# Kernel tuning notes

Measured on AMD Instinct MI355X. Metric: run time of the kernel, lower is better.

The kernel has to match this reference:

```python
import jax, jax.numpy as jnp
import numpy as np

QK_NOPE = 128  # qk_nope_head_dim; softmax scale uses nope+rope head dim
EPS = 1e-6

def _rmsnorm(x, w):
    return x * jax.lax.rsqrt(jnp.mean(x * x, axis=-1, keepdims=True) + EPS) * w

def _deinterleave(x):
    # torch: view(..., d//2, 2).transpose(-1, -2).reshape(..., d)
    return jnp.concatenate([x[..., 0::2], x[..., 1::2]], axis=-1)

def _rotate_half(x):
    h = x.shape[-1] // 2
    return jnp.concatenate([-x[..., h:], x[..., :h]], axis=-1)

def _rope_cos_sin(position_ids, dim, theta=10000.0):
    inv_freq = 1.0 / (theta ** (jnp.arange(0, dim, 2, dtype=jnp.float32) / dim))  # [dim/2]
    freqs = position_ids.astype(jnp.float32)[..., None] * inv_freq               # [B,S,dim/2]
    emb = jnp.concatenate([freqs, freqs], axis=-1)                               # [B,S,dim]
    return jnp.cos(emb)[:, None], jnp.sin(emb)[:, None]                          # [B,1,S,dim]


def setup_inputs() -> dict:
    B, S, HID, H = 2, 1024, 4096, 32
    QL, KVL, ROPE, V = 1536, 512, 64, 128
    key = jax.random.key(0)
    ks = jax.random.split(key, 8)
    def w(k, shape, fan_in):
        return jax.random.normal(k, shape, jnp.float32) * (fan_in ** -0.5)
    hidden_states = jax.random.normal(ks[0], (B, S, HID), jnp.float32)
    causal = jnp.tril(jnp.ones((S, S), bool))
    attention_mask = jnp.where(causal, 0.0, -1e9).astype(jnp.float32)[None, None]  # [1,1,S,S]
    position_ids = jnp.broadcast_to(jnp.arange(S, dtype=jnp.int32), (B, S))
    return {
        'hidden_states': hidden_states,
        'attention_mask': attention_mask,
        'position_ids': position_ids,
        'w_q_a': w(ks[1], (HID, QL), HID),
        'q_a_ln_w': jnp.ones((QL,), jnp.float32),
        'q_rope': w(ks[2], (QL, H * ROPE), QL),
        'fusedqk': w(ks[3], (H, QL, KVL), QL),
        'w_kv_a': w(ks[4], (HID, KVL + ROPE), HID),
        'kv_a_ln_w': jnp.ones((KVL,), jnp.float32),
        'per_head_v_up': w(ks[5], (H, KVL, V), KVL),
        'w_o': w(ks[6], (H * V, HID), H * V),
    }


def _mla_forward(hidden_states, attention_mask, position_ids, w_q_a, q_a_ln_w,
                 q_rope, fusedqk, w_kv_a, kv_a_ln_w, per_head_v_up, w_o):
    B, S, _ = hidden_states.shape
    H, QL, KVL = fusedqk.shape
    ROPE = q_rope.shape[1] // H
    # compressed KV projection (MQA): split into latent kv and rope key part
    ckv = hidden_states @ w_kv_a                              # [B,S,KVL+ROPE]
    kva = _rmsnorm(ckv[..., :KVL], kv_a_ln_w)                 # [B,S,KVL]
    k_pe = ckv[..., KVL:][:, None]                            # [B,1,S,ROPE]
    # low-rank query
    q_a = _rmsnorm(hidden_states @ w_q_a, q_a_ln_w)           # [B,S,QL]
    q_pe = (q_a @ q_rope).reshape(B, S, H, ROPE).transpose(0, 2, 1, 3)  # [B,H,S,ROPE]
    # interleaved RoPE (deinterleave then standard rotate-half)
    cos, sin = _rope_cos_sin(position_ids, ROPE)
    qd = _deinterleave(q_pe)
    kd = _deinterleave(k_pe)
    q_pe = qd * cos + _rotate_half(qd) * sin                  # [B,H,S,ROPE]
    k_pe = kd * cos + _rotate_half(kd) * sin                  # [B,1,S,ROPE]
    # absorbed query: q_a @ (q_up @ k_up^T), precomputed as fusedqk
    q_abs = jnp.einsum('bsr,hrc->bhsc', q_a, fusedqk)         # [B,H,S,KVL]
    query = jnp.concatenate([q_abs, q_pe], axis=-1)           # [B,H,S,KVL+ROPE]
    keys = jnp.concatenate([kva, k_pe[:, 0]], axis=-1)        # [B,S,KVL+ROPE]
    scale = (QK_NOPE + ROPE) ** -0.5
    scores = jnp.einsum('bhsd,btd->bhst', query, keys) * scale + attention_mask
    attn = jax.nn.softmax(scores, axis=-1)                    # [B,H,S,S]
    ctx = jnp.einsum('bhst,btc->bhsc', attn, kva)             # [B,H,S,KVL]
    out = jnp.einsum('bhsc,hcv->bhsv', ctx, per_head_v_up)    # [B,H,S,V]
    out = out.transpose(0, 2, 1, 3).reshape(B, S, -1)         # [B,S,H*V]
    return out @ w_o                                          # [B,S,HID]


def reference(hidden_states, attention_mask, position_ids, w_q_a, q_a_ln_w,
              q_rope, fusedqk, w_kv_a, kv_a_ln_w, per_head_v_up, w_o):
    return _mla_forward(hidden_states, attention_mask, position_ids, w_q_a,
                        q_a_ln_w, q_rope, fusedqk, w_kv_a, kv_a_ln_w,
                        per_head_v_up, w_o)
```

## Files before the change

### kernel.cpp

```cpp
#include <hip/hip_runtime.h>


typedef __attribute__((ext_vector_type(8))) short s16x8;
typedef __attribute__((ext_vector_type(4))) float f32x4;

__device__ __forceinline__ float bf2f(unsigned short u) {
  union { unsigned int i; float f; } v; v.i = ((unsigned int)u) << 16; return v.f;
}
__device__ __forceinline__ unsigned short f2bf(float f) {
  union { float f; unsigned int i; } v; v.f = f;
  unsigned int x = v.i;
  x += 0x7fffu + ((x >> 16) & 1u);
  return (unsigned short)(x >> 16);
}

__device__ __forceinline__ void async16(const unsigned short* g, unsigned short* l) {
  __builtin_amdgcn_global_load_lds(
      (const __attribute__((address_space(1))) unsigned int*)g,
      (__attribute__((address_space(3))) unsigned int*)l, 16, 0, 0);
}

__global__ __launch_bounds__(256) void conv_bf16(
    const float* __restrict__ s, unsigned short* __restrict__ d)
{
  const long long i = ((long long)blockIdx.x * 256 + threadIdx.x) * 8;
  float4 a = *(const float4*)(s + i);
  float4 b = *(const float4*)(s + i + 4);
  union { uint4 v; unsigned short u[8]; } o;
  o.u[0] = f2bf(a.x); o.u[1] = f2bf(a.y); o.u[2] = f2bf(a.z); o.u[3] = f2bf(a.w);
  o.u[4] = f2bf(b.x); o.u[5] = f2bf(b.y); o.u[6] = f2bf(b.z); o.u[7] = f2bf(b.w);
  *(uint4*)(d + i) = o.v;
}

__global__ __launch_bounds__(256) void transpose_w(
    const float* __restrict__ src, unsigned short* __restrict__ dst,
    int R, int C, long long sS, long long sD)
{
  __shared__ unsigned short tile[32][36];
  src += (long long)blockIdx.z * sS;
  dst += (long long)blockIdx.z * sD;
  const int c0 = blockIdx.x * 32, r0 = blockIdx.y * 32;
  const int tid = threadIdx.x;
  const int rr = tid >> 3, cc4 = (tid & 7) * 4;
  if (c0 < C) {
    float4 v = *(const float4*)(src + (long long)(r0 + rr) * C + c0 + cc4);
    tile[cc4 + 0][rr] = f2bf(v.x); tile[cc4 + 1][rr] = f2bf(v.y);
    tile[cc4 + 2][rr] = f2bf(v.z); tile[cc4 + 3][rr] = f2bf(v.w);
  } else {
#pragma unroll
    for (int j = 0; j < 4; ++j) tile[cc4 + j][rr] = 0;
  }
  __syncthreads();
  const int cr = tid >> 3, rc4 = (tid & 7) * 4;
  union { uint2 v; unsigned short u[4]; } o;
#pragma unroll
  for (int j = 0; j < 4; ++j) o.u[j] = tile[cr][rc4 + j];
  *(uint2*)(dst + (long long)(c0 + cr) * R + r0 + rc4) = o.v;
}

template<int ODT>
__global__ __launch_bounds__(256) void gemm128(
    const unsigned short* __restrict__ A, const unsigned short* __restrict__ Bt,
    void* __restrict__ Cv, int K, int lda, int ldb, int ldc, int batH,
    long long sAb, long long sAh, long long sBb, long long sBh,
    long long sCb, long long sCh)
{
  const int z = blockIdx.z;
  const int bz = z / batH, hz = z % batH;
  A  += (long long)bz * sAb + (long long)hz * sAh;
  Bt += (long long)bz * sBb + (long long)hz * sBh;
  const long long co = (long long)bz * sCb + (long long)hz * sCh;

  __shared__ __align__(16) unsigned short As[128 * 32];
  __shared__ __align__(16) unsigned short Bs[128 * 32];

  const int tid = threadIdx.x, w = tid >> 6, lane = tid & 63;
  const int quad = lane >> 4, ml = lane & 15;
  const int wm = (w >> 1) * 64, wn = (w & 1) * 64;
  const int m0 = blockIdx.y * 128, n0 = blockIdx.x * 128;

  const int r0 = tid >> 2, k8 = (tid & 3) * 8;
  const unsigned short* Ag0 = A  + (long long)(m0 + r0)      * lda + k8;
  const unsigned short* Ag1 = A  + (long long)(m0 + r0 + 64) * lda + k8;
  const unsigned short* Bg0 = Bt + (long long)(n0 + r0)      * ldb + k8;
  const unsigned short* Bg1 = Bt + (long long)(n0 + r0 + 64) * ldb + k8;
  unsigned short* la0 = &As[tid * 8];
  unsigned short* la1 = &As[(tid + 256) * 8];
  unsigned short* lb0 = &Bs[tid * 8];
  unsigned short* lb1 = &Bs[(tid + 256) * 8];

  f32x4 acc[4][4] = {};

  for (int k0 = 0; k0 < K; k0 += 32) {
    __syncthreads();
    async16(Ag0 + k0, la0);
    async16(Ag1 + k0, la1);
    async16(Bg0 + k0, lb0);
    async16(Bg1 + k0, lb1);
    __syncthreads();

    s16x8 af[4], bf[4];
#pragma unroll
    for (int mi = 0; mi < 4; ++mi)
      af[mi] = *(const s16x8*)(&As[(wm + mi * 16 + ml) * 32 + quad * 8]);
#pragma unroll
    for (int ni = 0; ni < 4; ++ni)
      bf[ni] = *(const s16x8*)(&Bs[(wn + ni * 16 + ml) * 32 + quad * 8]);
#pragma unroll
    for (int mi = 0; mi < 4; ++mi)
#pragma unroll
      for (int ni = 0; ni < 4; ++ni)
        acc[mi][ni] = __builtin_amdgcn_mfma_f32_16x16x32_bf16(af[mi], bf[ni], acc[mi][ni], 0, 0, 0);
  }

#pragma unroll
  for (int mi = 0; mi < 4; ++mi)
#pragma unroll
    for (int ni = 0; ni < 4; ++ni)
#pragma unroll
      for (int r = 0; r < 4; ++r) {
        const int row = m0 + wm + mi * 16 + quad * 4 + r;
        const int col = n0 + wn + ni * 16 + ml;
        if (ODT)
          ((unsigned short*)Cv)[co + (long long)row * ldc + col] = f2bf(acc[mi][ni][r]);
        else
          ((float*)Cv)[co + (long long)row * ldc + col] = acc[mi][ni][r];
      }
}

__global__ __launch_bounds__(256) void kv_norm_rope(
    const float* __restrict__ qckv, const float* __restrict__ w,
    const int* __restrict__ pos_ids, unsigned short* __restrict__ keys)
{
  __shared__ float sbuf[4];
  const int r = blockIdx.x, tid = threadIdx.x;
  const float* row = qckv + (long long)r * 2176 + 1536;
  float x0 = row[tid], x1 = row[256 + tid];
  float ss = x0 * x0 + x1 * x1;
#pragma unroll
  for (int o = 32; o; o >>= 1) ss += __shfl_xor(ss, o);
  if ((tid & 63) == 0) sbuf[tid >> 6] = ss;
  __syncthreads();
  const float tot = sbuf[0] + sbuf[1] + sbuf[2] + sbuf[3];
  const float rms = rsqrtf(tot / 512.0f + 1e-6f);
  unsigned short* kr = keys + (long long)r * 576;
  kr[tid]       = f2bf(x0 * rms * w[tid]);
  kr[256 + tid] = f2bf(x1 * rms * w[256 + tid]);
  if (tid < 32) {
    const float pos = (float)pos_ids[r];
    const float invf = exp2f(-0.41524101186098287f * (float)tid);
    float sn, c; sincosf(pos * invf, &sn, &c);
    const float a0 = row[512 + 2 * tid], a1 = row[512 + 2 * tid + 1];
    kr[512 + tid] = f2bf(a0 * c - a1 * sn);
    kr[544 + tid] = f2bf(a1 * c + a0 * sn);
  }
}

__global__ __launch_bounds__(256) void q_norm(
    const float* __restrict__ qckv, const float* __restrict__ w,
    unsigned short* __restrict__ qa_bf)
{
  __shared__ float sbuf[4];
  const int r = blockIdx.x, tid = threadIdx.x;
  const float* row = qckv + (long long)r * 2176;
  float x[6]; float ss = 0.f;
#pragma unroll
  for (int j = 0; j < 6; ++j) { x[j] = row[tid + 256 * j]; ss += x[j] * x[j]; }
#pragma unroll
  for (int o = 32; o; o >>= 1) ss += __shfl_xor(ss, o);
  if ((tid & 63) == 0) sbuf[tid >> 6] = ss;
  __syncthreads();
  const float tot = sbuf[0] + sbuf[1] + sbuf[2] + sbuf[3];
  const float rms = rsqrtf(tot / 1536.0f + 1e-6f);
#pragma unroll
  for (int j = 0; j < 6; ++j) {
    const int idx = tid + 256 * j;
    qa_bf[(long long)r * 1536 + idx] = f2bf(x[j] * rms * w[idx]);
  }
}

__global__ __launch_bounds__(256) void rope_q(
    const unsigned short* __restrict__ qpe, const int* __restrict__ pos_ids,
    unsigned short* __restrict__ query)
{
  const int r = blockIdx.x;
  const int b = r >> 10, s = r & 1023;
  const float pos = (float)pos_ids[r];
  for (int p = threadIdx.x; p < 1024; p += 256) {
    const int h = p >> 5, i = p & 31;
    const float invf = exp2f(-0.41524101186098287f * (float)i);
    float sn, c; sincosf(pos * invf, &sn, &c);
    const float a0 = bf2f(qpe[(long long)r * 2048 + h * 64 + 2 * i]);
    const float a1 = bf2f(qpe[(long long)r * 2048 + h * 64 + 2 * i + 1]);
    const long long qrow = ((long long)(b * 32 + h) * 1024 + s) * 576;
    query[qrow + 512 + i] = f2bf(a0 * c - a1 * sn);
    query[qrow + 544 + i] = f2bf(a1 * c + a0 * sn);
  }
}

__global__ __launch_bounds__(256) void transpose_keys(
    const unsigned short* __restrict__ keys, unsigned short* __restrict__ keysT)
{
  __shared__ unsigned short tile[32][36];
  const int tid = threadIdx.x;
  const int t0 = blockIdx.x * 32, d0 = blockIdx.y * 32, b = blockIdx.z;
  const int r = tid >> 3, c4 = (tid & 7) * 4;
  *(uint2*)(&tile[r][c4]) =
      *(const uint2*)(keys + ((long long)(b * 1024 + t0 + r) * 576 + d0 + c4));
  __syncthreads();
  unsigned short v[4];
#pragma unroll
  for (int j = 0; j < 4; ++j) v[j] = tile[c4 + j][r];
  *(uint2*)(keysT + ((long long)(b * 512 + d0 + r) * 1024 + t0 + c4)) = *(uint2*)v;
}

__global__ __launch_bounds__(512, 2) void flash_mfma(
    const unsigned short* __restrict__ query,
    const unsigned short* __restrict__ keys,
    const unsigned short* __restrict__ keysT,
    unsigned short* __restrict__ ctx)
{
  __shared__ __align__(16) unsigned short Ks[2][32 * 640];
  __shared__ __align__(16) unsigned short Ps[2][8][640];
  __shared__ float alpha_s[2][128];
  __shared__ float l_s[128];
  __shared__ __align__(16) int rflag[2][8];

  const int tid = threadIdx.x, w = tid >> 6, lane = tid & 63;
  const int quad = lane >> 4, ml = lane & 15;
  const int bid = blockIdx.x;
  const int bh = bid & 63;
  const int qt = 7 - (bid >> 6);
  const int q0 = qt * 128;
  const int b = bh >> 5;
  const float scale = 0.07216878364870323f;

  const unsigned short* kb  = keys  + (long long)b * 1024 * 576;
  const unsigned short* vtb = keysT + (long long)b * 512 * 1024;

  const unsigned short* qg =
      query + ((long long)bh * 1024 + q0 + w * 16 + ml) * 576 + quad * 8;
  s16x8 qf[18];
#pragma unroll
  for (int ks = 0; ks < 18; ++ks) qf[ks] = *(const s16x8*)(qg + ks * 32);

  int koff[5];
#pragma unroll
  for (int j = 0; j < 5; ++j) {
    const int idx = tid + 512 * j;
    const int row = idx / 80;
    const int c16 = idx - row * 80;
    koff[j] = row * 576 + ((c16 ^ (row & 7)) << 3);
  }
  char* ldsb = (char*)&Ks[0][0] + tid * 16;
  auto stage = [&](int t, int buf) {
    const long long toff = (long long)t * 18432;
    char* lb = ldsb + buf * 40960;
#pragma unroll
    for (int j = 0; j < 5; ++j)
      async16(kb + toff + koff[j], (unsigned short*)(lb + j * 8192));
  };

  const int e3 = ml & 7;
  const int qi = q0 + w * 16 + ml;
  const int ntile = 4 * qt + 4;

  float m = -1e30f, l = 0.f;
  f32x4 o[8][4] = {};

  stage(0, 0);

  for (int ti = 0; ti < ntile; ++ti) {
    const int buf = ti & 1;
    const int t0 = ti * 32;

    if (ti + 1 < ntile) {
      stage(ti + 1, buf ^ 1);
      asm volatile("s_waitcnt vmcnt(5)" ::: "memory");
    } else {
      asm volatile("s_waitcnt vmcnt(0)" ::: "memory");
    }
    __builtin_amdgcn_sched_barrier(0);
    __builtin_amdgcn_s_barrier();
    __builtin_amdgcn_sched_barrier(0);

    const bool wdead = (t0 > q0 + w * 16 + 15);
    if (!wdead) {
      const unsigned short* Kb = &Ks[buf][0];
      f32x4 sc0 = {}, sc1 = {};
#pragma unroll
      for (int ks = 0; ks < 18; ++ks) {
        const int xr = ((ks * 4 + quad) ^ e3) << 3;
        s16x8 k0 = *(const s16x8*)(Kb + ml * 640 + xr);
        s16x8 k1 = *(const s16x8*)(Kb + (16 + ml) * 640 + xr);
        sc0 = __builtin_amdgcn_mfma_f32_16x16x32_bf16(k0, qf[ks], sc0, 0, 0, 0);
        sc1 = __builtin_amdgcn_mfma_f32_16x16x32_bf16(k1, qf[ks], sc1, 0, 0, 0);
      }

      float p[8]; float mx = -1e30f;
      const bool tail = (t0 + 31 > q0 + w * 16);
#pragma unroll
      for (int r = 0; r < 4; ++r) {
        float v0 = sc0[r] * scale, v1 = sc1[r] * scale;
        if (tail) {
          if (t0 + quad * 4 + r > qi)      v0 = -1e30f;
          if (t0 + 16 + quad * 4 + r > qi) v1 = -1e30f;
        }
        p[r] = v0; p[4 + r] = v1;
        mx = fmaxf(mx, fmaxf(v0, v1));
      }
      mx = fmaxf(mx, __shfl_xor(mx, 16));
      mx = fmaxf(mx, __shfl_xor(mx, 32));

      float alpha = 1.0f;
      int resc = 0;
      if (!__all(mx - m <= 8.0f)) {
        const float mn = fmaxf(m, mx);
        alpha = __expf(m - mn);
        m = mn;
        l *= alpha;
        resc = 1;
      }
      if (lane == 0) rflag[buf][w] = resc;
      if (quad == 0) alpha_s[buf][w * 16 + ml] = alpha;

      float ps = 0.f;
#pragma unroll
      for (int j = 0; j < 8; ++j) { p[j] = __expf(p[j] - m); ps += p[j]; }
      ps += __shfl_xor(ps, 16);
      ps += __shfl_xor(ps, 32);
      l += ps;

#pragma unroll
      for (int c = 0; c < 2; ++c) {
        union { unsigned short u[4]; uint2 v; } pk;
        pk.u[0] = f2bf(p[c * 4 + 0]); pk.u[1] = f2bf(p[c * 4 + 1]);
        pk.u[2] = f2bf(p[c * 4 + 2]); pk.u[3] = f2bf(p[c * 4 + 3]);
        *(uint2*)(&Ps[buf][w][ml * 40 + c * 16 + quad * 4]) = pk.v;
      }
    } else {
      if (lane == 0) rflag[buf][w] = 0;
      if (quad == 0) alpha_s[buf][w * 16 + ml] = 1.0f;
    }

    const unsigned short* vg =
        vtb + (long long)(w * 64 + ml) * 1024 + t0 + quad * 8;
    s16x8 vf[4];
#pragma unroll
    for (int nt = 0; nt < 4; ++nt) vf[nt] = *(const s16x8*)(vg + nt * 16 * 1024);

    asm volatile("s_waitcnt lgkmcnt(0)" ::: "memory");
    __builtin_amdgcn_sched_barrier(0);
    __builtin_amdgcn_s_barrier();
    __builtin_amdgcn_sched_barrier(0);

    const int4 ra = *(const int4*)&rflag[buf][0];
    const int4 rb = *(const int4*)&rflag[buf][4];
    if (ra.x | ra.y | ra.z | ra.w | rb.x | rb.y | rb.z | rb.w) {
#pragma unroll
      for (int qc = 0; qc < 8; ++qc)
#pragma unroll
        for (int r = 0; r < 4; ++r) {
          const float a = alpha_s[buf][qc * 16 + quad * 4 + r];
#pragma unroll
          for (int nt = 0; nt < 4; ++nt) o[qc][nt][r] *= a;
        }
    }

#pragma unroll
    for (int qc = 0; qc < 8; ++qc) {
      if (t0 > q0 + qc * 16 + 15) continue;
      s16x8 pa = *(const s16x8*)(&Ps[buf][qc][ml * 40 + quad * 8]);
#pragma unroll
      for (int nt = 0; nt < 4; ++nt)
        o[qc][nt] = __builtin_amdgcn_mfma_f32_16x16x32_bf16(pa, vf[nt], o[qc][nt], 0, 0, 0);
    }
  }

  if (quad == 0) l_s[w * 16 + ml] = l;
  __syncthreads();

  unsigned short* cb = ctx + ((long long)bh * 1024 + q0) * 512 + w * 64 + ml;
#pragma unroll
  for (int qc = 0; qc < 8; ++qc)
#pragma unroll
    for (int r = 0; r < 4; ++r) {
      const float linv = 1.0f / l_s[qc * 16 + quad * 4 + r];
      unsigned short* crow = cb + (long long)(qc * 16 + quad * 4 + r) * 512;
#pragma unroll
      for (int nt = 0; nt < 4; ++nt)
        crow[nt * 16] = f2bf(o[qc][nt][r] * linv);
    }
}

extern "C" void kernel_launch(void* const* d_in, const int* in_sizes, int n_in,
                              void* d_out, int out_size, void* d_ws, size_t ws_size,
                              hipStream_t stream)
{
  (void)in_sizes; (void)n_in; (void)out_size; (void)ws_size;
  const float* hs      = (const float*)d_in[0];
  const int*   pos     = (const int*)d_in[2];
  const float* w_q_a   = (const float*)d_in[3];
  const float* q_a_ln  = (const float*)d_in[4];
  const float* q_rope  = (const float*)d_in[5];
  const float* fusedqk = (const float*)d_in[6];
  const float* w_kv_a  = (const float*)d_in[7];
  const float* kv_ln   = (const float*)d_in[8];
  const float* v_up    = (const float*)d_in[9];
  const float* w_o     = (const float*)d_in[10];
  char* ws = (char*)d_ws;

  unsigned short* woT    = (unsigned short*)(ws + 0);
  unsigned short* vupT   = (unsigned short*)(ws + 33554432);
  unsigned short* keys   = (unsigned short*)(ws + 37748736);
  unsigned short* keysT  = (unsigned short*)(ws + 40108032);
  unsigned short* ctx    = (unsigned short*)(ws + 42205184);
  unsigned short* fqkT   = (unsigned short*)(ws + 42205184);
  unsigned short* qab    = (unsigned short*)(ws + 92536832);
  unsigned short* qpe    = (unsigned short*)(ws + 99828288);
  unsigned short* hsb    = (unsigned short*)(ws + 92536832);
  unsigned short* query  = (unsigned short*)(ws + 109314048);
  unsigned short* wqkvT  = (unsigned short*)(ws + 109314048);
  unsigned short* qropeT = (unsigned short*)(ws + 127139840);
  float*          qckv   = (float*)(ws + 133431296);
  unsigned short* outh   = (unsigned short*)(ws + 109314048);

  const dim3 blk(256);

  conv_bf16<<<dim3(4096), blk, 0, stream>>>(hs, hsb);
  transpose_w<<<dim3(48, 128, 1), blk, 0, stream>>>(w_q_a, wqkvT, 4096, 1536, 0, 0);
  transpose_w<<<dim3(20, 128, 1), blk, 0, stream>>>(w_kv_a, wqkvT + (long long)1536 * 4096,
      4096, 576, 0, 0);
  transpose_w<<<dim3(64, 48, 1), blk, 0, stream>>>(q_rope, qropeT, 1536, 2048, 0, 0);
  transpose_w<<<dim3(16, 48, 32), blk, 0, stream>>>(fusedqk, fqkT, 1536, 512,
      (long long)1536 * 512, (long long)512 * 1536);
  transpose_w<<<dim3(4, 16, 32), blk, 0, stream>>>(v_up, vupT, 512, 128,
      (long long)512 * 128, (long long)128 * 512);
  transpose_w<<<dim3(128, 128, 1), blk, 0, stream>>>(w_o, woT, 4096, 4096, 0, 0);

  gemm128<0><<<dim3(17, 16, 1), blk, 0, stream>>>(hsb, wqkvT, (void*)qckv,
      4096, 4096, 4096, 2176, 1, 0, 0, 0, 0, 0, 0);
  kv_norm_rope<<<dim3(2048), blk, 0, stream>>>(qckv, kv_ln, pos, keys);
  transpose_keys<<<dim3(32, 16, 2), blk, 0, stream>>>(keys, keysT);
  q_norm<<<dim3(2048), blk, 0, stream>>>(qckv, q_a_ln, qab);
  gemm128<1><<<dim3(16, 16, 1), blk, 0, stream>>>(qab, qropeT, (void*)qpe,
      1536, 1536, 1536, 2048, 1, 0, 0, 0, 0, 0, 0);
  rope_q<<<dim3(2048), blk, 0, stream>>>(qpe, pos, query);
  gemm128<1><<<dim3(4, 8, 64), blk, 0, stream>>>(qab, fqkT, (void*)query,
      1536, 1536, 1536, 576, 32,
      (long long)1024 * 1536, 0, 0, (long long)512 * 1536,
      (long long)32 * 1024 * 576, (long long)1024 * 576);
  flash_mfma<<<dim3(512), dim3(512), 0, stream>>>(query, keys, keysT, ctx);
  gemm128<1><<<dim3(1, 8, 64), blk, 0, stream>>>(ctx, vupT, (void*)outh,
      512, 512, 512, 4096, 32,
      (long long)32 * 1024 * 512, (long long)1024 * 512, 0, (long long)128 * 512,
      (long long)1024 * 4096, 128);
  gemm128<0><<<dim3(32, 16, 1), blk, 0, stream>>>(outh, woT, d_out,
      4096, 4096, 4096, 4096, 1, 0, 0, 0, 0, 0, 0);
}
```

Baseline: 904.9 us.

## Have each wave own its query rows across full latent dim in flash attention

Restructures the PV step so each wave accumulates output for its own 16 query rows over all 512 latent columns, instead of each wave owning a 64-column slice for all 128 rows. This removes the cross-wave sharing of P, rescale factors and flags through LDS, along with the second block barrier per tile, and lets fully masked waves skip the whole tile. The cost is that every wave now reads the full V tile from global memory, so V traffic per block is eight times higher. The K prefetch is also moved to after the barrier with a full vmcnt(0) wait, which reduces overlap between loading and compute.

New measurement: 1.092 ms. 20.6% more time.

```diff
diff --git a/kernel.cpp b/kernel.cpp
--- a/kernel.cpp
+++ b/kernel.cpp
@@ -221,10 +221,7 @@
     unsigned short* __restrict__ ctx)
 {
   __shared__ __align__(16) unsigned short Ks[2][32 * 640];
-  __shared__ __align__(16) unsigned short Ps[2][8][640];
-  __shared__ float alpha_s[2][128];
-  __shared__ float l_s[128];
-  __shared__ __align__(16) int rflag[2][8];
+  __shared__ __align__(16) unsigned short Ps[8][16 * 40];
 
   const int tid = threadIdx.x, w = tid >> 6, lane = tid & 63;
   const int quad = lane >> 4, ml = lane & 15;
@@ -266,7 +263,7 @@
   const int ntile = 4 * qt + 4;
 
   float m = -1e30f, l = 0.f;
-  f32x4 o[8][4] = {};
+  f32x4 o[32] = {};
 
   stage(0, 0);
 
@@ -274,123 +271,95 @@
     const int buf = ti & 1;
     const int t0 = ti * 32;
 
-    if (ti + 1 < ntile) {
-      stage(ti + 1, buf ^ 1);
-      asm volatile("s_waitcnt vmcnt(5)" ::: "memory");
-    } else {
-      asm volatile("s_waitcnt vmcnt(0)" ::: "memory");
-    }
+    asm volatile("s_waitcnt vmcnt(0)" ::: "memory");
     __builtin_amdgcn_sched_barrier(0);
     __builtin_amdgcn_s_barrier();
     __builtin_amdgcn_sched_barrier(0);
-
-    const bool wdead = (t0 > q0 + w * 16 + 15);
-    if (!wdead) {
-      const unsigned short* Kb = &Ks[buf][0];
-      f32x4 sc0 = {}, sc1 = {};
-#pragma unroll
-      for (int ks = 0; ks < 18; ++ks) {
-        const int xr = ((ks * 4 + quad) ^ e3) << 3;
-        s16x8 k0 = *(const s16x8*)(Kb + ml * 640 + xr);
-        s16x8 k1 = *(const s16x8*)(Kb + (16 + ml) * 640 + xr);
-        sc0 = __builtin_amdgcn_mfma_f32_16x16x32_bf16(k0, qf[ks], sc0, 0, 0, 0);
-        sc1 = __builtin_amdgcn_mfma_f32_16x16x32_bf16(k1, qf[ks], sc1, 0, 0, 0);
+    if (ti + 1 < ntile) stage(ti + 1, buf ^ 1);
+
+    if (t0 > q0 + w * 16 + 15) continue;
+
+    const unsigned short* Kb = &Ks[buf][0];
+    f32x4 sc0 = {}, sc1 = {};
+#pragma unroll
+    for (int ks = 0; ks < 18; ++ks) {
+      const int xr = ((ks * 4 + quad) ^ e3) << 3;
+      s16x8 k0 = *(const s16x8*)(Kb + ml * 640 + xr);
+      s16x8 k1 = *(const s16x8*)(Kb + (16 + ml) * 640 + xr);
+      sc0 = __builtin_amdgcn_mfma_f32_16x16x32_bf16(k0, qf[ks], sc0, 0, 0, 0);
+      sc1 = __builtin_amdgcn_mfma_f32_16x16x32_bf16(k1, qf[ks], sc1, 0, 0, 0);
+    }
+
+    float p[8]; float mx = -1e30f;
+    const bool tail = (t0 + 31 > q0 + w * 16);
+#pragma unroll
+    for (int r = 0; r < 4; ++r) {
+      float v0 = sc0[r] * scale, v1 = sc1[r] * scale;
+      if (tail) {
+        if (t0 + quad * 4 + r > qi)      v0 = -1e30f;
+        if (t0 + 16 + quad * 4 + r > qi) v1 = -1e30f;
       }
-
-      float p[8]; float mx = -1e30f;
-      const bool tail = (t0 + 31 > q0 + w * 16);
-#pragma unroll
-      for (int r = 0; r < 4; ++r) {
-        float v0 = sc0[r] * scale, v1 = sc1[r] * scale;
-        if (tail) {
-          if (t0 + quad * 4 + r > qi)      v0 = -1e30f;
-          if (t0 + 16 + quad * 4 + r > qi) v1 = -1e30f;
-        }
-        p[r] = v0; p[4 + r] = v1;
-        mx = fmaxf(mx, fmaxf(v0, v1));
-      }
-      mx = fmaxf(mx, __shfl_xor(mx, 16));
-      mx = fmaxf(mx, __shfl_xor(mx, 32));
-
-      float alpha = 1.0f;
-      int resc = 0;
-      if (!__all(mx - m <= 8.0f)) {
-        const float mn = fmaxf(m, mx);
-        alpha = __expf(m - mn);
-        m = mn;
-        l *= alpha;
-        resc = 1;
-      }
-      if (lane == 0) rflag[buf][w] = resc;
-      if (quad == 0) alpha_s[buf][w * 16 + ml] = alpha;
-
-      float ps = 0.f;
-#pragma unroll
-      for (int j = 0; j < 8; ++j) { p[j] = __expf(p[j] - m); ps += p[j]; }
-      ps += __shfl_xor(ps, 16);
-      ps += __shfl_xor(ps, 32);
-      l += ps;
-
-#pragma unroll
-      for (int c = 0; c < 2; ++c) {
-        union { unsigned short u[4]; uint2 v; } pk;
-        pk.u[0] = f2bf(p[c * 4 + 0]); pk.u[1] = f2bf(p[c * 4 + 1]);
-        pk.u[2] = f2bf(p[c * 4 + 2]); pk.u[3] = f2bf(p[c * 4 + 3]);
-        *(uint2*)(&Ps[buf][w][ml * 40 + c * 16 + quad * 4]) = pk.v;
-      }
-    } else {
-      if (lane == 0) rflag[buf][w] = 0;
-      if (quad == 0) alpha_s[buf][w * 16 + ml] = 1.0f;
+      p[r] = v0; p[4 + r] = v1;
+      mx = fmaxf(mx, fmaxf(v0, v1));
     }
-
-    const unsigned short* vg =
-        vtb + (long long)(w * 64 + ml) * 1024 + t0 + quad * 8;
-    s16x8 vf[4];
-#pragma unroll
-    for (int nt = 0; nt < 4; ++nt) vf[nt] = *(const s16x8*)(vg + nt * 16 * 1024);
-
+    mx = fmaxf(mx, __shfl_xor(mx, 16));
+    mx = fmaxf(mx, __shfl_xor(mx, 32));
+
+    const bool keep = (mx - m <= 8.0f);
+    const float alpha = keep ? 1.0f : __expf(m - mx);
+    m = keep ? m : mx;
+
+    float ps = 0.f;
+#pragma unroll
+    for (int j = 0; j < 8; ++j) { p[j] = __expf(p[j] - m); ps += p[j]; }
+    ps += __shfl_xor(ps, 16);
+    ps += __shfl_xor(ps, 32);
+    l = l * alpha + ps;
+
+#pragma unroll
+    for (int c = 0; c < 2; ++c) {
+      union { unsigned short u[4]; uint2 v; } pk;
+      pk.u[0] = f2bf(p[c * 4 + 0]); pk.u[1] = f2bf(p[c * 4 + 1]);
+      pk.u[2] = f2bf(p[c * 4 + 2]); pk.u[3] = f2bf(p[c * 4 + 3]);
+      *(uint2*)(&Ps[w][ml * 40 + c * 16 + quad * 4]) = pk.v;
+    }
     asm volatile("s_waitcnt lgkmcnt(0)" ::: "memory");
     __builtin_amdgcn_sched_barrier(0);
-    __builtin_amdgcn_s_barrier();
-    __builtin_amdgcn_sched_barrier(0);
-
-    const int4 ra = *(const int4*)&rflag[buf][0];
-    const int4 rb = *(const int4*)&rflag[buf][4];
-    if (ra.x | ra.y | ra.z | ra.w | rb.x | rb.y | rb.z | rb.w) {
-#pragma unroll
-      for (int qc = 0; qc < 8; ++qc)
-#pragma unroll
-        for (int r = 0; r < 4; ++r) {
-          const float a = alpha_s[buf][qc * 16 + quad * 4 + r];
-#pragma unroll
-          for (int nt = 0; nt < 4; ++nt) o[qc][nt][r] *= a;
-        }
+    s16x8 pa = *(const s16x8*)(&Ps[w][ml * 40 + quad * 8]);
+
+    if (!__all(keep)) {
+      float ar[4];
+#pragma unroll
+      for (int r = 0; r < 4; ++r) ar[r] = __shfl(alpha, 4 * quad + r);
+#pragma unroll
+      for (int nt = 0; nt < 32; ++nt)
+#pragma unroll
+        for (int r = 0; r < 4; ++r) o[nt][r] *= ar[r];
     }
 
-#pragma unroll
-    for (int qc = 0; qc < 8; ++qc) {
-      if (t0 > q0 + qc * 16 + 15) continue;
-      s16x8 pa = *(const s16x8*)(&Ps[buf][qc][ml * 40 + quad * 8]);
-#pragma unroll
-      for (int nt = 0; nt < 4; ++nt)
-        o[qc][nt] = __builtin_amdgcn_mfma_f32_16x16x32_bf16(pa, vf[nt], o[qc][nt], 0, 0, 0);
+    const unsigned short* vg = vtb + (long long)ml * 1024 + t0 + quad * 8;
+#pragma unroll
+    for (int g = 0; g < 4; ++g) {
+      s16x8 vf[8];
+#pragma unroll
+      for (int j = 0; j < 8; ++j)
+        vf[j] = *(const s16x8*)(vg + (long long)(g * 8 + j) * 16 * 1024);
+#pragma unroll
+      for (int j = 0; j < 8; ++j)
+        o[g * 8 + j] = __builtin_amdgcn_mfma_f32_16x16x32_bf16(pa, vf[j], o[g * 8 + j], 0, 0, 0);
     }
   }
 
-  if (quad == 0) l_s[w * 16 + ml] = l;
-  __syncthreads();
-
-  unsigned short* cb = ctx + ((long long)bh * 1024 + q0) * 512 + w * 64 + ml;
-#pragma unroll
-  for (int qc = 0; qc < 8; ++qc)
-#pragma unroll
-    for (int r = 0; r < 4; ++r) {
-      const float linv = 1.0f / l_s[qc * 16 + quad * 4 + r];
-      unsigned short* crow = cb + (long long)(qc * 16 + quad * 4 + r) * 512;
-#pragma unroll
-      for (int nt = 0; nt < 4; ++nt)
-        crow[nt * 16] = f2bf(o[qc][nt][r] * linv);
-    }
+  float linv[4];
+#pragma unroll
+  for (int r = 0; r < 4; ++r) linv[r] = 1.0f / __shfl(l, 4 * quad + r);
+
+  unsigned short* cb = ctx + ((long long)bh * 1024 + q0 + w * 16) * 512 + ml;
+#pragma unroll
+  for (int nt = 0; nt < 32; ++nt)
+#pragma unroll
+    for (int r = 0; r < 4; ++r)
+      cb[(long long)(quad * 4 + r) * 512 + nt * 16] = f2bf(o[nt][r] * linv[r]);
 }
 
 extern "C" void kernel_launch(void* const* d_in, const int* in_sizes, int n_in,
```
